# Optimization experiments

Hardware: AMD Instinct MI355X
Metric: run time of the kernel (lower is better)

Reference implementation:

```python
import jax, jax.numpy as jnp
import numpy as np

B, C, T = 32, 64, 4096
K = 256  # truncated memory length (kwargs['k'])


def setup_inputs() -> dict:
    key = jax.random.key(0)
    k1, k2 = jax.random.split(key)
    x = jax.random.normal(k1, (B, C, T), dtype=jnp.float32)
    epsilon = jax.random.normal(k2, (), dtype=jnp.float32)
    loc = jnp.asarray(0.5, dtype=jnp.float32)    # alpha_loc parameter
    scale = jnp.asarray(0.1, dtype=jnp.float32)  # alpha_scale parameter (pre-softplus)
    return {"x": x, "loc": loc, "scale": scale, "epsilon": epsilon, "k": K}


def _gl_coeffs(alpha, k, dtype):
    # Grunwald-Letnikov weights: w_0 = 1, w_j = w_{j-1} * (j - 1 - alpha) / j
    j = jnp.arange(k, dtype=dtype)
    factors = jnp.where(j == 0, jnp.asarray(1.0, dtype),
                        (j - 1.0 - alpha) / jnp.maximum(j, 1.0))
    return jnp.cumprod(factors)  # [k]


def reference(x, loc, scale, epsilon, k):
    # reparameterized fractional order (Normal prior): alpha = loc + softplus(scale) * eps
    alpha = loc + jax.nn.softplus(scale) * epsilon
    w = _gl_coeffs(alpha, k, x.dtype)  # [k]
    b, c, t = x.shape
    # truncated GL fractional derivative = causal depthwise conv with k taps:
    # out[n] = sum_{j=0}^{k-1} w_j * x[n-j]
    lhs = x.reshape(b * c, 1, t)                 # [N, 1, T]
    rhs = w[::-1].reshape(1, 1, k)               # [O=1, I=1, K] (flip for correlation)
    out = jax.lax.conv_general_dilated(lhs, rhs, window_strides=(1,),
                                       padding=[(k - 1, 0)])
    return out.reshape(b, c, t)
```

## Files before the change

### kernel.cpp

```cpp
#include <hip/hip_runtime.h>
#include <hip/hip_bf16.h>
#include <hip/hip_fp16.h>

#define TLEN 4096
#define KTAPS 256
#define NT 18
#define WCH 32

typedef __attribute__((ext_vector_type(8))) unsigned short ushort8v;
typedef __attribute__((ext_vector_type(8))) _Float16 f16x8;
typedef __attribute__((ext_vector_type(4))) unsigned int uint4v;
typedef __attribute__((ext_vector_type(16))) float f32x16;

__global__ void __launch_bounds__(256, 4)
frac_conv_fused(const float* __restrict__ x,
                const float* __restrict__ loc,
                const float* __restrict__ scale,
                const float* __restrict__ eps,
                float* __restrict__ out) {
    __shared__ float s[KTAPS];
    __shared__ unsigned int wrevp[320];
    __shared__ __align__(16) unsigned short Bf[WCH * 64 * 8];

    const int tid  = threadIdx.x;
    const int wave = tid >> 6;
    const int lane = tid & 63;
    const int l5   = lane >> 5;
    const int ln   = lane & 31;

    int rt, sg;
    if ((gridDim.x & 127) == 0) {
        const int nrt  = gridDim.x >> 4;
        const int xcd  = blockIdx.x & 7;
        const int slot = blockIdx.x >> 3;
        rt = xcd * (nrt >> 3) + (slot >> 4);
        sg = slot & 15;
    } else {
        rt = blockIdx.x >> 4;
        sg = blockIdx.x & 15;
    }
    const int bn0 = sg * 256;

    const int r  = tid >> 3;
    const int cg = tid & 7;
    const float* __restrict__ xrow = x + (size_t)(rt * 32 + r) * TLEN;
    float4 v[16];
    #pragma unroll
    for (int jj = 0; jj < 16; ++jj) {
        const int w0 = cg * 4 + jj * 32;
        const int tg = bn0 - 256 + w0;
        v[jj] = (tg >= 0) ? *(const float4*)(xrow + tg) : make_float4(0.f, 0.f, 0.f, 0.f);
    }

    const float alpha = loc[0] + log1pf(expf(scale[0])) * eps[0];
    {
        const float f = (tid == 0) ? 1.0f : (((float)tid - 1.0f - alpha) / (float)tid);
        s[tid] = f;
        __syncthreads();
        #pragma unroll
        for (int st = 1; st < KTAPS; st <<= 1) {
            const float vv = s[tid];
            const float p  = (tid >= st) ? s[tid - st] : 1.0f;
            __syncthreads();
            s[tid] = vv * p;
            __syncthreads();
        }
    }

    {
        const int j = tid;
        const float a = (j >= 32) ? s[287 - j] : 0.0f;
        const float b = (j >= 31 && j <= 286) ? s[286 - j] : 0.0f;
        wrevp[j] = __builtin_bit_cast(unsigned int, __builtin_amdgcn_cvt_pkrtz(a, b));
        if (tid < 64) {
            const int j2 = 256 + tid;
            const float a2 = (j2 <= 287) ? s[287 - j2] : 0.0f;
            const float b2 = (j2 <= 286) ? s[286 - j2] : 0.0f;
            wrevp[j2] = __builtin_bit_cast(unsigned int, __builtin_amdgcn_cvt_pkrtz(a2, b2));
        }
    }

    {
        uint2* Bf2 = (uint2*)Bf;
        #pragma unroll
        for (int jj = 0; jj < 16; ++jj) {
            const int w0 = cg * 4 + jj * 32;
            const auto a = __builtin_amdgcn_cvt_pkrtz(v[jj].x, v[jj].y);
            const auto b = __builtin_amdgcn_cvt_pkrtz(v[jj].z, v[jj].w);
            const int c  = w0 >> 4;
            const int h8 = (w0 >> 3) & 1;
            const int e0 = w0 & 7;
            const int uoff = (c * 64 + r + 32 * h8) * 8 + e0;
            Bf2[uoff >> 2] = make_uint2(__builtin_bit_cast(unsigned int, a),
                                        __builtin_bit_cast(unsigned int, b));
        }
    }
    __syncthreads();

    const int n0  = bn0 + wave * 64;
    const int lcb = wave * 4;
    const f16x8* Bv = (const f16x8*)Bf;
    const int o0 = 31 - ln + 8 * l5;

    auto LOADA = [&](int d) -> f16x8 {
        const int o = o0 + 16 * d;
        uint4v u;
        u[0] = wrevp[o];
        u[1] = wrevp[o + 2];
        u[2] = wrevp[o + 4];
        u[3] = wrevp[o + 6];
        return __builtin_bit_cast(f16x8, u);
    };

    f16x8 Afr[NT];
    f16x8 Bfr[NT + 2];
    Bfr[0] = Bv[(lcb + 0) * 64 + lane];
    Bfr[1] = Bv[(lcb + 1) * 64 + lane];
    Bfr[2] = Bv[(lcb + 2) * 64 + lane];
    Bfr[3] = Bv[(lcb + 3) * 64 + lane];
    Afr[0] = LOADA(0);
    Afr[1] = LOADA(1);

    f32x16 acc0 = {0.f, 0.f, 0.f, 0.f, 0.f, 0.f, 0.f, 0.f,
                   0.f, 0.f, 0.f, 0.f, 0.f, 0.f, 0.f, 0.f};
    f32x16 acc1 = acc0;

    #pragma unroll
    for (int d = 0; d < NT; ++d) {
        if (d + 4 < NT + 2) Bfr[d + 4] = Bv[(lcb + d + 4) * 64 + lane];
        if (d + 2 < NT)     Afr[d + 2] = LOADA(d + 2);
        acc0 = __builtin_amdgcn_mfma_f32_32x32x16_f16(Afr[d], Bfr[d],     acc0, 0, 0, 0);
        acc1 = __builtin_amdgcn_mfma_f32_32x32x16_f16(Afr[d], Bfr[d + 2], acc1, 0, 0, 0);
    }

    float* __restrict__ orow = out + (size_t)(rt * 32 + ln) * TLEN;
    #pragma unroll
    for (int g = 0; g < 4; ++g) {
        *(float4*)(orow + n0 + 8 * g + 4 * l5) =
            make_float4(acc0[4 * g + 0], acc0[4 * g + 1], acc0[4 * g + 2], acc0[4 * g + 3]);
        *(float4*)(orow + n0 + 32 + 8 * g + 4 * l5) =
            make_float4(acc1[4 * g + 0], acc1[4 * g + 1], acc1[4 * g + 2], acc1[4 * g + 3]);
    }
}

__global__ void gl_coeff_kernel(const float* __restrict__ loc,
                                const float* __restrict__ scale,
                                const float* __restrict__ eps,
                                float* __restrict__ w_out) {
    __shared__ float s[KTAPS];
    const int j = threadIdx.x;
    const float alpha = loc[0] + log1pf(expf(scale[0])) * eps[0];
    float f = (j == 0) ? 1.0f : (((float)j - 1.0f - alpha) / (float)j);
    s[j] = f;
    __syncthreads();
    #pragma unroll
    for (int st = 1; st < KTAPS; st <<= 1) {
        float v = s[j];
        float p = (j >= st) ? s[j - st] : 1.0f;
        __syncthreads();
        s[j] = v * p;
        __syncthreads();
    }
    w_out[j] = s[j];
}

__global__ void __launch_bounds__(256)
frac_conv_kernel(const float* __restrict__ x,
                 const float* __restrict__ w,
                 float* __restrict__ out) {
    __shared__ __align__(16) float xs[KTAPS + TLEN];
    __shared__ __align__(16) float wl[KTAPS];
    const int row = blockIdx.x;
    const int tid = threadIdx.x;
    const float* __restrict__ xr = x + (size_t)row * TLEN;
    float* __restrict__ orow = out + (size_t)row * TLEN;
    if (tid < 64) ((float4*)xs)[tid] = make_float4(0.f, 0.f, 0.f, 0.f);
    float4* xs4w = (float4*)(xs + KTAPS);
    const float4* xr4 = (const float4*)xr;
    #pragma unroll
    for (int k = 0; k < 4; ++k) xs4w[tid + k * 256] = xr4[tid + k * 256];
    if (tid < 64) ((float4*)wl)[tid] = ((const float4*)w)[tid];
    __syncthreads();
    const float4* __restrict__ xsv = (const float4*)xs;
    float4 acc[4]; float4 lo[4], hi[4]; int n0[4];
    #pragma unroll
    for (int g = 0; g < 4; ++g) {
        n0[g] = (tid << 2) + (g << 10);
        acc[g] = make_float4(0.f, 0.f, 0.f, 0.f);
        const int c = n0[g] >> 2;
        hi[g] = xsv[64 + c];
        lo[g] = xsv[63 + c];
    }
    #pragma unroll 4
    for (int j = 0; j < KTAPS - 4; j += 4) {
        const float4 w4 = *(const float4*)(wl + j);
        #pragma unroll
        for (int g = 0; g < 4; ++g) {
            acc[g].x += w4.x*hi[g].x + w4.y*lo[g].w + w4.z*lo[g].z + w4.w*lo[g].y;
            acc[g].y += w4.x*hi[g].y + w4.y*hi[g].x + w4.z*lo[g].w + w4.w*lo[g].z;
            acc[g].z += w4.x*hi[g].z + w4.y*hi[g].y + w4.z*hi[g].x + w4.w*lo[g].w;
            acc[g].w += w4.x*hi[g].w + w4.y*hi[g].z + w4.z*hi[g].y + w4.w*hi[g].x;
            hi[g] = lo[g];
            lo[g] = xsv[64 + ((n0[g] - j - 8) >> 2)];
        }
    }
    {
        const float4 w4 = *(const float4*)(wl + (KTAPS - 4));
        #pragma unroll
        for (int g = 0; g < 4; ++g) {
            acc[g].x += w4.x*hi[g].x + w4.y*lo[g].w + w4.z*lo[g].z + w4.w*lo[g].y;
            acc[g].y += w4.x*hi[g].y + w4.y*hi[g].x + w4.z*lo[g].w + w4.w*lo[g].z;
            acc[g].z += w4.x*hi[g].z + w4.y*hi[g].y + w4.z*hi[g].x + w4.w*lo[g].w;
            acc[g].w += w4.x*hi[g].w + w4.y*hi[g].z + w4.z*hi[g].y + w4.w*hi[g].x;
        }
    }
    #pragma unroll
    for (int g = 0; g < 4; ++g) *(float4*)(orow + n0[g]) = acc[g];
}

extern "C" void kernel_launch(void* const* d_in, const int* in_sizes, int n_in,
                              void* d_out, int out_size, void* d_ws, size_t ws_size,
                              hipStream_t stream) {
    const float* x     = (const float*)d_in[0];
    const float* loc   = (const float*)d_in[1];
    const float* scale = (const float*)d_in[2];
    const float* eps   = (const float*)d_in[3];
    float* out = (float*)d_out;
    const int rows = in_sizes[0] / TLEN;

    if ((rows % 32) == 0) {
        frac_conv_fused<<<(rows / 32) * 16, 256, 0, stream>>>(x, loc, scale, eps, out);
    } else {
        float* w = (float*)d_ws;
        gl_coeff_kernel<<<1, 256, 0, stream>>>(loc, scale, eps, w);
        frac_conv_kernel<<<rows, 256, 0, stream>>>(x, w, out);
    }
}
```

Measured before the change: 18.81 us.

## Halve output tile per block, double grid, and use wave-shuffle coefficient scan

Each block now computes 128 output samples per 32-row tile instead of 256. That doubles the grid to 2048 blocks and shrinks shared memory and registers, so occupancy hint rises to 5 waves per SIMD. The goal is more parallelism and better latency hiding. In exchange, the 256-sample halo load becomes a larger fraction of each block's input, so redundant global reads and fp16 conversion work grow. The Grunwald-Letnikov cumprod now uses a per-lane 4-element product plus a wavefront shuffle scan, replacing the 8-step shared-memory scan with its many barriers. The XCD block remapping is also simplified to a generic chunked mapping.

```diff
diff --git a/kernel.cpp b/kernel.cpp
--- a/kernel.cpp
+++ b/kernel.cpp
@@ -5,20 +5,19 @@
 #define TLEN 4096
 #define KTAPS 256
 #define NT 18
-#define WCH 32
-
-typedef __attribute__((ext_vector_type(8))) unsigned short ushort8v;
+#define WCH 24
+
 typedef __attribute__((ext_vector_type(8))) _Float16 f16x8;
 typedef __attribute__((ext_vector_type(4))) unsigned int uint4v;
 typedef __attribute__((ext_vector_type(16))) float f32x16;
 
-__global__ void __launch_bounds__(256, 4)
-frac_conv_fused(const float* __restrict__ x,
-                const float* __restrict__ loc,
-                const float* __restrict__ scale,
-                const float* __restrict__ eps,
-                float* __restrict__ out) {
-    __shared__ float s[KTAPS];
+__global__ void __launch_bounds__(256, 5)
+frac_conv_fused2(const float* __restrict__ x,
+                 const float* __restrict__ loc,
+                 const float* __restrict__ scale,
+                 const float* __restrict__ eps,
+                 float* __restrict__ out) {
+    __shared__ __align__(16) float s[KTAPS];
     __shared__ unsigned int wrevp[320];
     __shared__ __align__(16) unsigned short Bf[WCH * 64 * 8];
 
@@ -28,49 +27,52 @@
     const int l5   = lane >> 5;
     const int ln   = lane & 31;
 
-    int rt, sg;
-    if ((gridDim.x & 127) == 0) {
-        const int nrt  = gridDim.x >> 4;
-        const int xcd  = blockIdx.x & 7;
-        const int slot = blockIdx.x >> 3;
-        rt = xcd * (nrt >> 3) + (slot >> 4);
-        sg = slot & 15;
-    } else {
-        rt = blockIdx.x >> 4;
-        sg = blockIdx.x & 15;
-    }
-    const int bn0 = sg * 256;
+    int wgid = blockIdx.x;
+    if ((gridDim.x & 7) == 0) {
+        const int cpx = gridDim.x >> 3;
+        wgid = (blockIdx.x & 7) * cpx + (blockIdx.x >> 3);
+    }
+    const int rt  = wgid >> 5;
+    const int sg  = wgid & 31;
+    const int bn0 = sg * 128;
 
     const int r  = tid >> 3;
     const int cg = tid & 7;
     const float* __restrict__ xrow = x + (size_t)(rt * 32 + r) * TLEN;
-    float4 v[16];
-    #pragma unroll
-    for (int jj = 0; jj < 16; ++jj) {
+    float4 v[12];
+    #pragma unroll
+    for (int jj = 0; jj < 12; ++jj) {
         const int w0 = cg * 4 + jj * 32;
         const int tg = bn0 - 256 + w0;
         v[jj] = (tg >= 0) ? *(const float4*)(xrow + tg) : make_float4(0.f, 0.f, 0.f, 0.f);
     }
 
-    const float alpha = loc[0] + log1pf(expf(scale[0])) * eps[0];
-    {
-        const float f = (tid == 0) ? 1.0f : (((float)tid - 1.0f - alpha) / (float)tid);
-        s[tid] = f;
-        __syncthreads();
-        #pragma unroll
-        for (int st = 1; st < KTAPS; st <<= 1) {
-            const float vv = s[tid];
-            const float p  = (tid >= st) ? s[tid - st] : 1.0f;
-            __syncthreads();
-            s[tid] = vv * p;
-            __syncthreads();
-        }
-    }
+    {
+        const float alpha = loc[0] + log1pf(expf(scale[0])) * eps[0];
+        const int j0 = 4 * lane;
+        const float f0 = (j0 == 0) ? 1.0f : (((float)j0 - 1.0f - alpha) / (float)j0);
+        const float f1 = (((float)j0 + 0.0f - alpha) / (float)(j0 + 1));
+        const float f2 = (((float)j0 + 1.0f - alpha) / (float)(j0 + 2));
+        const float f3 = (((float)j0 + 2.0f - alpha) / (float)(j0 + 3));
+        const float p0 = f0, p1 = p0 * f1, p2 = p1 * f2, p3 = p2 * f3;
+        float g = p3;
+        #pragma unroll
+        for (int dlt = 1; dlt < 64; dlt <<= 1) {
+            const float t = __shfl_up(g, dlt, 64);
+            if (lane >= dlt) g *= t;
+        }
+        float Sprev = __shfl_up(g, 1, 64);
+        if (lane == 0) Sprev = 1.0f;
+        if (wave == 0) {
+            ((float4*)s)[lane] = make_float4(Sprev * p0, Sprev * p1, Sprev * p2, g);
+        }
+    }
+    __syncthreads();
 
     {
         const int j = tid;
         const float a = (j >= 32) ? s[287 - j] : 0.0f;
-        const float b = (j >= 31 && j <= 286) ? s[286 - j] : 0.0f;
+        const float b = (j >= 31) ? s[286 - j] : 0.0f;
         wrevp[j] = __builtin_bit_cast(unsigned int, __builtin_amdgcn_cvt_pkrtz(a, b));
         if (tid < 64) {
             const int j2 = 256 + tid;
@@ -83,7 +85,7 @@
     {
         uint2* Bf2 = (uint2*)Bf;
         #pragma unroll
-        for (int jj = 0; jj < 16; ++jj) {
+        for (int jj = 0; jj < 12; ++jj) {
             const int w0 = cg * 4 + jj * 32;
             const auto a = __builtin_amdgcn_cvt_pkrtz(v[jj].x, v[jj].y);
             const auto b = __builtin_amdgcn_cvt_pkrtz(v[jj].z, v[jj].w);
@@ -97,8 +99,8 @@
     }
     __syncthreads();
 
-    const int n0  = bn0 + wave * 64;
-    const int lcb = wave * 4;
+    const int n0  = bn0 + wave * 32;
+    const int lcb = wave * 2;
     const f16x8* Bv = (const f16x8*)Bf;
     const int o0 = 31 - ln + 8 * l5;
 
@@ -113,7 +115,7 @@
     };
 
     f16x8 Afr[NT];
-    f16x8 Bfr[NT + 2];
+    f16x8 Bfr[NT];
     Bfr[0] = Bv[(lcb + 0) * 64 + lane];
     Bfr[1] = Bv[(lcb + 1) * 64 + lane];
     Bfr[2] = Bv[(lcb + 2) * 64 + lane];
@@ -121,25 +123,21 @@
     Afr[0] = LOADA(0);
     Afr[1] = LOADA(1);
 
-    f32x16 acc0 = {0.f, 0.f, 0.f, 0.f, 0.f, 0.f, 0.f, 0.f,
-                   0.f, 0.f, 0.f, 0.f, 0.f, 0.f, 0.f, 0.f};
-    f32x16 acc1 = acc0;
+    f32x16 acc = {0.f, 0.f, 0.f, 0.f, 0.f, 0.f, 0.f, 0.f,
+                  0.f, 0.f, 0.f, 0.f, 0.f, 0.f, 0.f, 0.f};
 
     #pragma unroll
     for (int d = 0; d < NT; ++d) {
-        if (d + 4 < NT + 2) Bfr[d + 4] = Bv[(lcb + d + 4) * 64 + lane];
-        if (d + 2 < NT)     Afr[d + 2] = LOADA(d + 2);
-        acc0 = __builtin_amdgcn_mfma_f32_32x32x16_f16(Afr[d], Bfr[d],     acc0, 0, 0, 0);
-        acc1 = __builtin_amdgcn_mfma_f32_32x32x16_f16(Afr[d], Bfr[d + 2], acc1, 0, 0, 0);
+        if (d + 4 < NT) Bfr[d + 4] = Bv[(lcb + d + 4) * 64 + lane];
+        if (d + 2 < NT) Afr[d + 2] = LOADA(d + 2);
+        acc = __builtin_amdgcn_mfma_f32_32x32x16_f16(Afr[d], Bfr[d], acc, 0, 0, 0);
     }
 
     float* __restrict__ orow = out + (size_t)(rt * 32 + ln) * TLEN;
     #pragma unroll
     for (int g = 0; g < 4; ++g) {
         *(float4*)(orow + n0 + 8 * g + 4 * l5) =
-            make_float4(acc0[4 * g + 0], acc0[4 * g + 1], acc0[4 * g + 2], acc0[4 * g + 3]);
-        *(float4*)(orow + n0 + 32 + 8 * g + 4 * l5) =
-            make_float4(acc1[4 * g + 0], acc1[4 * g + 1], acc1[4 * g + 2], acc1[4 * g + 3]);
+            make_float4(acc[4 * g + 0], acc[4 * g + 1], acc[4 * g + 2], acc[4 * g + 3]);
     }
 }
 
@@ -229,7 +227,7 @@
     const int rows = in_sizes[0] / TLEN;
 
     if ((rows % 32) == 0) {
-        frac_conv_fused<<<(rows / 32) * 16, 256, 0, stream>>>(x, loc, scale, eps, out);
+        frac_conv_fused2<<<(rows / 32) * 32, 256, 0, stream>>>(x, loc, scale, eps, out);
     } else {
         float* w = (float*)d_ws;
         gl_coeff_kernel<<<1, 256, 0, stream>>>(loc, scale, eps, w);
```

New measurement: 19.77 us. 5.1% more time.
